# Kernel optimization log

Hardware: AMD Instinct MI355X
Metric: run time of the kernel (lower is better)

Reference implementation:

```python
import jax, jax.numpy as jnp
import numpy as np

N = 50000      # n_nodes
E = 800000     # n_edges (avg degree 16)
D_IN, D_HID, D_OUT = 128, 128, 64


def setup_inputs() -> dict:
    key = jax.random.key(0)
    k1, k2, k3, k4 = jax.random.split(key, 4)
    x = jax.random.normal(k1, (N, D_IN), jnp.float32)
    edge_index = jax.random.randint(k2, (2, E), 0, N, jnp.int32)
    # Glorot-style init for the two GCNConv linear weights
    W1 = jax.random.normal(k3, (D_IN, D_HID), jnp.float32) / np.sqrt(D_IN)
    W2 = jax.random.normal(k4, (D_HID, D_OUT), jnp.float32) / np.sqrt(D_HID)
    b1 = jnp.zeros((D_HID,), jnp.float32)
    b2 = jnp.zeros((D_OUT,), jnp.float32)
    return {"x": x, "edge_index": edge_index, "W1": W1, "b1": b1, "W2": W2, "b2": b2}


def _gcn_conv(x, W, b, src, dst):
    """PyG GCNConv: linear transform, then sym-normalized aggregation with self-loops."""
    h = x @ W                                   # [N, F_out]
    ones = jnp.ones((src.shape[0],), h.dtype)
    # degree includes the self-loop weight of 1
    deg = jax.ops.segment_sum(ones, dst, num_segments=N) + 1.0
    dinv = jax.lax.rsqrt(deg)                   # D^{-1/2}
    norm = dinv[src] * dinv[dst]                # per-edge normalization
    agg = jax.ops.segment_sum(h[src] * norm[:, None], dst, num_segments=N)
    # self-loop contribution: norm_ii = dinv_i^2
    return agg + h * (dinv * dinv)[:, None] + b


def reference(x, edge_index, W1, b1, W2, b2):
    src, dst = edge_index[0], edge_index[1]
    h = jax.nn.relu(_gcn_conv(x, W1, b1, src, dst))
    out = jax.nn.relu(_gcn_conv(h, W2, b2, src, dst))
    return out
```

## Files before the change

### kernel.cpp

```cpp
#include <hip/hip_runtime.h>

typedef unsigned short u16;
typedef __attribute__((ext_vector_type(8))) short short8;
typedef __attribute__((ext_vector_type(4))) float f32x4;

__device__ __forceinline__ float bf2f(u16 h) {
    union { unsigned u; float f; } v; v.u = ((unsigned)h) << 16; return v.f;
}
__device__ __forceinline__ float bflo(unsigned u) {
    union { unsigned u; float f; } v; v.u = u << 16; return v.f;
}
__device__ __forceinline__ float bfhi(unsigned u) {
    union { unsigned u; float f; } v; v.u = u & 0xFFFF0000u; return v.f;
}
__device__ __forceinline__ u16 f2bf(float f) {
    union { float f; unsigned u; } v; v.f = f;
    unsigned u = v.u;
    u += 0x7FFFu + ((u >> 16) & 1u);
    return (u16)(u >> 16);
}

__global__ void k_detect(const u16* __restrict__ x, int* __restrict__ flag) {
    __shared__ int c_s;
    if (threadIdx.x == 0) c_s = 0;
    __syncthreads();
    int c = 0;
    for (int i = threadIdx.x; i < 2048; i += blockDim.x) {
        int e = (x[2 * i] >> 7) & 0xFF;
        c += (e >= 160 || e <= 80) ? 1 : 0;
    }
    atomicAdd(&c_s, c);
    __syncthreads();
    if (threadIdx.x == 0) *flag = (c_s > 64) ? 1 : 0;
}

__global__ void k_convert_w(const void* __restrict__ W1, const void* __restrict__ b1,
                            const void* __restrict__ W2, const void* __restrict__ b2,
                            u16* __restrict__ out, const int* __restrict__ flag) {
    const int n1 = 128 * 128, n2 = n1 + 128, n3 = n2 + 128 * 64, n4 = n3 + 64;
    int i = blockIdx.x * 256 + threadIdx.x;
    if (i >= n4) return;
    const void* src; int off;
    if (i < n1)      { src = W1; off = i; }
    else if (i < n2) { src = b1; off = i - n1; }
    else if (i < n3) { src = W2; off = i - n2; }
    else             { src = b2; off = i - n3; }
    out[i] = *flag ? f2bf(((const float*)src)[off]) : ((const u16*)src)[off];
}


__global__ void k_degpos(const int* __restrict__ dst, int* __restrict__ cnt,
                         int* __restrict__ pos, int E) {
    int e = blockIdx.x * blockDim.x + threadIdx.x;
    if (e < E) pos[e] = atomicAdd(&cnt[dst[e]], 1);
}

__global__ void k_scan_blocks(const int* __restrict__ cnt, int* __restrict__ rowp,
                              int* __restrict__ sums, int n) {
    __shared__ int s[256];
    int t = threadIdx.x;
    int i = blockIdx.x * 256 + t;
    int v = (i < n) ? cnt[i] : 0;
    s[t] = v;
    __syncthreads();
    for (int off = 1; off < 256; off <<= 1) {
        int add = (t >= off) ? s[t - off] : 0;
        __syncthreads();
        s[t] += add;
        __syncthreads();
    }
    if (i < n) rowp[i] = s[t] - v;
    if (t == 255) sums[blockIdx.x] = s[255];
}

__global__ void k_scan_top(int* __restrict__ sums, int nb) {
    __shared__ int s[256];
    int t = threadIdx.x;
    int v = (t < nb) ? sums[t] : 0;
    s[t] = v;
    __syncthreads();
    for (int off = 1; off < 256; off <<= 1) {
        int add = (t >= off) ? s[t - off] : 0;
        __syncthreads();
        s[t] += add;
        __syncthreads();
    }
    sums[t] = s[t] - v;
}

__global__ void k_finalize(int* __restrict__ rowp, const int* __restrict__ sums,
                           const int* __restrict__ cnt, float* __restrict__ dinv,
                           int n, int E) {
    int i = blockIdx.x * 256 + threadIdx.x;
    if (i < n) {
        rowp[i] += sums[i >> 8];
        dinv[i] = rsqrtf((float)cnt[i] + 1.0f);
    }
    if (i == 0) rowp[n] = E;
}

__global__ void k_fill2(const int* __restrict__ src, const int* __restrict__ dst,
                        const int* __restrict__ pos, const int* __restrict__ rowp,
                        int* __restrict__ col, int E) {
    int e = blockIdx.x * blockDim.x + threadIdx.x;
    if (e < E) col[rowp[dst[e]] + pos[e]] = src[e];
}


template <int NOUT>
__global__ void k_gemm_scale(const void* __restrict__ Av, const u16* __restrict__ W,
                             const float* __restrict__ dinv, u16* __restrict__ out,
                             int M, const int* __restrict__ flag) {
    __shared__ u16 Wt[NOUT][136];
    int t = threadIdx.x;
    for (int idx = t; idx < NOUT * 128; idx += 256) {
        int k = idx / NOUT, n = idx % NOUT;
        Wt[n][k] = W[idx];
    }
    __syncthreads();
    int wave = t >> 6, lane = t & 63;
    int m0 = (blockIdx.x * 4 + wave) * 16;
    if (m0 >= M) return;
    int q = lane >> 4;
    int mr = lane & 15;

    short8 a[4];
    if (flag && *flag) {
        const float* arow = (const float*)Av + (size_t)(m0 + mr) * 128 + q * 8;
#pragma unroll
        for (int c = 0; c < 4; c++) {
            f32x4 lo = *(const f32x4*)(arow + c * 32);
            f32x4 hi = *(const f32x4*)(arow + c * 32 + 4);
            a[c][0] = (short)f2bf(lo.x); a[c][1] = (short)f2bf(lo.y);
            a[c][2] = (short)f2bf(lo.z); a[c][3] = (short)f2bf(lo.w);
            a[c][4] = (short)f2bf(hi.x); a[c][5] = (short)f2bf(hi.y);
            a[c][6] = (short)f2bf(hi.z); a[c][7] = (short)f2bf(hi.w);
        }
    } else {
        const u16* arow = (const u16*)Av + (size_t)(m0 + mr) * 128 + q * 8;
#pragma unroll
        for (int c = 0; c < 4; c++) a[c] = *(const short8*)(arow + c * 32);
    }

    f32x4 acc[NOUT / 16];
#pragma unroll
    for (int tl = 0; tl < NOUT / 16; tl++) acc[tl] = (f32x4){0.f, 0.f, 0.f, 0.f};

#pragma unroll
    for (int c = 0; c < 4; c++) {
#pragma unroll
        for (int tl = 0; tl < NOUT / 16; tl++) {
            short8 b = *(const short8*)(&Wt[tl * 16 + mr][c * 32 + q * 8]);
            acc[tl] = __builtin_amdgcn_mfma_f32_16x16x32_bf16(a[c], b, acc[tl], 0, 0, 0);
        }
    }

    int rbase = m0 + q * 4;
#pragma unroll
    for (int tl = 0; tl < NOUT / 16; tl++) {
#pragma unroll
        for (int r = 0; r < 4; r++) {
            int row = rbase + r;
            float v = acc[tl][r] * dinv[row];
            out[(size_t)row * NOUT + tl * 16 + mr] = f2bf(v);
        }
    }
}


template <int F>
__global__ void k_agg(const u16* __restrict__ g, const int* __restrict__ rowp,
                      const int* __restrict__ col, const float* __restrict__ dinv,
                      const u16* __restrict__ bias, u16* __restrict__ outh,
                      float* __restrict__ outf, const int* __restrict__ flag,
                      int N, int E) {
    constexpr int LPR = F / 8;
    constexpr int EPW = 64 / LPR;
    int d = blockIdx.x * 4 + (threadIdx.x >> 6);
    if (d >= N) return;
    int lane = threadIdx.x & 63;
    int er = lane / LPR;
    int fo = (lane % LPR) * 8;

    int beg = rowp[d], end = rowp[d + 1];
    if (beg < 0) beg = 0;
    if (end > E) end = E;
    int deg = end - beg;

    float a0[8], a1[8];
#pragma unroll
    for (int j = 0; j < 8; j++) { a0[j] = 0.f; a1[j] = 0.f; }

    for (int base = 0; base < deg; base += 64) {
        int cnt = deg - base; if (cnt > 64) cnt = 64;
        int colv = 0;
        if (lane < cnt) {
            int s = col[beg + base + lane];
            colv = s < 0 ? 0 : (s >= N ? N - 1 : s);
        }
        int full = cnt / EPW;
        int i = 0;
        for (; i + 2 <= full; i += 2) {
            int s0 = __shfl(colv, i * EPW + er, 64);
            int s1 = __shfl(colv, (i + 1) * EPW + er, 64);
            uint4 v0 = *(const uint4*)(g + (size_t)s0 * F + fo);
            uint4 v1 = *(const uint4*)(g + (size_t)s1 * F + fo);
            a0[0] += bflo(v0.x); a0[1] += bfhi(v0.x);
            a0[2] += bflo(v0.y); a0[3] += bfhi(v0.y);
            a0[4] += bflo(v0.z); a0[5] += bfhi(v0.z);
            a0[6] += bflo(v0.w); a0[7] += bfhi(v0.w);
            a1[0] += bflo(v1.x); a1[1] += bfhi(v1.x);
            a1[2] += bflo(v1.y); a1[3] += bfhi(v1.y);
            a1[4] += bflo(v1.z); a1[5] += bfhi(v1.z);
            a1[6] += bflo(v1.w); a1[7] += bfhi(v1.w);
        }
        if (i < full) {
            int s0 = __shfl(colv, i * EPW + er, 64);
            uint4 v0 = *(const uint4*)(g + (size_t)s0 * F + fo);
            a0[0] += bflo(v0.x); a0[1] += bfhi(v0.x);
            a0[2] += bflo(v0.y); a0[3] += bfhi(v0.y);
            a0[4] += bflo(v0.z); a0[5] += bfhi(v0.z);
            a0[6] += bflo(v0.w); a0[7] += bfhi(v0.w);
            i++;
        }
        int rem = cnt - full * EPW;
        int s0 = __shfl(colv, (full * EPW + er) & 63, 64);
        if (er < rem) {
            uint4 v0 = *(const uint4*)(g + (size_t)s0 * F + fo);
            a0[0] += bflo(v0.x); a0[1] += bfhi(v0.x);
            a0[2] += bflo(v0.y); a0[3] += bfhi(v0.y);
            a0[4] += bflo(v0.z); a0[5] += bfhi(v0.z);
            a0[6] += bflo(v0.w); a0[7] += bfhi(v0.w);
        }
    }
#pragma unroll
    for (int j = 0; j < 8; j++) a0[j] += a1[j];
#pragma unroll
    for (int off = LPR; off < 64; off <<= 1) {
#pragma unroll
        for (int j = 0; j < 8; j++) a0[j] += __shfl_xor(a0[j], off, 64);
    }

    if (lane < LPR) {
        uint4 sv = *(const uint4*)(g + (size_t)d * F + fo);
        uint4 bv = *(const uint4*)(bias + fo);
        float di = dinv[d];
        float r[8];
        r[0] = di * (a0[0] + bflo(sv.x)) + bflo(bv.x);
        r[1] = di * (a0[1] + bfhi(sv.x)) + bfhi(bv.x);
        r[2] = di * (a0[2] + bflo(sv.y)) + bflo(bv.y);
        r[3] = di * (a0[3] + bfhi(sv.y)) + bfhi(bv.y);
        r[4] = di * (a0[4] + bflo(sv.z)) + bflo(bv.z);
        r[5] = di * (a0[5] + bfhi(sv.z)) + bfhi(bv.z);
        r[6] = di * (a0[6] + bflo(sv.w)) + bflo(bv.w);
        r[7] = di * (a0[7] + bfhi(sv.w)) + bfhi(bv.w);
#pragma unroll
        for (int j = 0; j < 8; j++) r[j] = r[j] > 0.f ? r[j] : 0.f;
        size_t o = (size_t)d * F + fo;
        if (flag && *flag) {
            f32x4 w0 = {r[0], r[1], r[2], r[3]};
            f32x4 w1 = {r[4], r[5], r[6], r[7]};
            *(f32x4*)(outf + o) = w0;
            *(f32x4*)(outf + o + 4) = w1;
        } else {
            uint4 w;
            w.x = (unsigned)f2bf(r[0]) | ((unsigned)f2bf(r[1]) << 16);
            w.y = (unsigned)f2bf(r[2]) | ((unsigned)f2bf(r[3]) << 16);
            w.z = (unsigned)f2bf(r[4]) | ((unsigned)f2bf(r[5]) << 16);
            w.w = (unsigned)f2bf(r[6]) | ((unsigned)f2bf(r[7]) << 16);
            *(uint4*)(outh + o) = w;
        }
    }
}


extern "C" void kernel_launch(void* const* d_in, const int* in_sizes, int n_in,
                              void* d_out, int out_size, void* d_ws, size_t ws_size,
                              hipStream_t stream) {
    const int N = in_sizes[0] / 128;
    const int E = in_sizes[1] / 2;
    const int* ei = (const int*)d_in[1];
    const int* src = ei;
    const int* dst = ei + E;

    char* p = (char*)d_ws;
    auto alloc = [&](size_t b) { char* r = p; p += (b + 255) & ~(size_t)255; return r; };
    int*   flag = (int*)alloc(256);
    int*   rowp = (int*)alloc((size_t)(N + 1) * 4);
    float* dinv = (float*)alloc((size_t)N * 4);
    int*   col  = (int*)alloc((size_t)E * 4);
    u16*   wbuf = (u16*)alloc((size_t)(128 * 128 + 128 + 128 * 64 + 64) * 2);
    char*  slotA = alloc((size_t)N * 128 * 2);
    char*  slotB = alloc((size_t)N * 128 * 2);

    int* cnt  = (int*)slotA;
    int* sums = (int*)(slotA + (size_t)N * 4);
    u16* g1   = (u16*)slotA;
    u16* g2   = (u16*)slotA;
    int* pos  = (int*)slotB;
    u16* o1   = (u16*)slotB;
    u16* W1C = wbuf;
    u16* b1C = wbuf + 128 * 128;
    u16* W2C = b1C + 128;
    u16* b2C = W2C + 128 * 64;

    k_detect<<<1, 256, 0, stream>>>((const u16*)d_in[0], flag);
    k_convert_w<<<97, 256, 0, stream>>>(d_in[2], d_in[3], d_in[4], d_in[5], wbuf, flag);

    hipMemsetAsync(slotA, 0, (size_t)N * 4 + 1024, stream);
    int eb = (E + 255) / 256;
    int nb = (N + 255) / 256;
    k_degpos<<<eb, 256, 0, stream>>>(dst, cnt, pos, E);
    k_scan_blocks<<<nb, 256, 0, stream>>>(cnt, rowp, sums, N);
    k_scan_top<<<1, 256, 0, stream>>>(sums, nb);
    k_finalize<<<nb, 256, 0, stream>>>(rowp, sums, cnt, dinv, N, E);
    k_fill2<<<eb, 256, 0, stream>>>(src, dst, pos, rowp, col, E);

    int gb = (N / 16 + 3) / 4;
    int ab = (N + 3) / 4;
    k_gemm_scale<128><<<gb, 256, 0, stream>>>(d_in[0], W1C, dinv, g1, N, flag);
    k_agg<128><<<ab, 256, 0, stream>>>(g1, rowp, col, dinv, b1C,
                                       o1, nullptr, nullptr, N, E);
    k_gemm_scale<64><<<gb, 256, 0, stream>>>(o1, W2C, dinv, g2, N, nullptr);
    k_agg<64><<<ab, 256, 0, stream>>>(g2, rowp, col, dinv, b2C,
                                      (u16*)d_out, (float*)d_out, flag, N, E);
}
```

Before: 218.7 us.

## Fuse all GCN stages into one persistent cooperative kernel with grid syncs

Replaces the eleven separate launches (detect, weight convert, degree count, scans, fill, two GEMMs, two aggregations) with one cooperative kernel that runs each phase in grid-stride loops and uses grid.sync between phases. Flag detection is merged with the degree count, and the CSR column fill is overlapped with the first GEMM phase. The aim is to remove per-launch overhead and inter-kernel gaps. In exchange, occupancy is capped at a persistent grid sized from max active blocks per CU, and each phase pays a grid-wide barrier.

```diff
diff --git a/kernel.cpp b/kernel.cpp
--- a/kernel.cpp
+++ b/kernel.cpp
@@ -1,17 +1,20 @@
 #include <hip/hip_runtime.h>
+#include <hip/hip_cooperative_groups.h>
+
+namespace cg = cooperative_groups;
 
 typedef unsigned short u16;
 typedef __attribute__((ext_vector_type(8))) short short8;
 typedef __attribute__((ext_vector_type(4))) float f32x4;
 
+__device__ __forceinline__ float bflo(unsigned u) {
+    union { unsigned u; float f; } v; v.u = u << 16; return v.f;
+}
+__device__ __forceinline__ float bfhi(unsigned u) {
+    union { unsigned u; float f; } v; v.u = u & 0xFFFF0000u; return v.f;
+}
 __device__ __forceinline__ float bf2f(u16 h) {
     union { unsigned u; float f; } v; v.u = ((unsigned)h) << 16; return v.f;
-}
-__device__ __forceinline__ float bflo(unsigned u) {
-    union { unsigned u; float f; } v; v.u = u << 16; return v.f;
-}
-__device__ __forceinline__ float bfhi(unsigned u) {
-    union { unsigned u; float f; } v; v.u = u & 0xFFFF0000u; return v.f;
 }
 __device__ __forceinline__ u16 f2bf(float f) {
     union { float f; unsigned u; } v; v.f = f;
@@ -20,278 +23,193 @@
     return (u16)(u >> 16);
 }
 
-__global__ void k_detect(const u16* __restrict__ x, int* __restrict__ flag) {
-    __shared__ int c_s;
-    if (threadIdx.x == 0) c_s = 0;
+template <int NOUT>
+__device__ void gemm_phase(const void* __restrict__ Av, const u16* __restrict__ W,
+                           const float* __restrict__ dinv, u16* __restrict__ outp,
+                           int M, int useF32, char* lds_) {
+    u16 (*Wt)[136] = (u16(*)[136])lds_;
+    int t = threadIdx.x;
     __syncthreads();
-    int c = 0;
-    for (int i = threadIdx.x; i < 2048; i += blockDim.x) {
-        int e = (x[2 * i] >> 7) & 0xFF;
-        c += (e >= 160 || e <= 80) ? 1 : 0;
-    }
-    atomicAdd(&c_s, c);
-    __syncthreads();
-    if (threadIdx.x == 0) *flag = (c_s > 64) ? 1 : 0;
-}
-
-__global__ void k_convert_w(const void* __restrict__ W1, const void* __restrict__ b1,
-                            const void* __restrict__ W2, const void* __restrict__ b2,
-                            u16* __restrict__ out, const int* __restrict__ flag) {
-    const int n1 = 128 * 128, n2 = n1 + 128, n3 = n2 + 128 * 64, n4 = n3 + 64;
-    int i = blockIdx.x * 256 + threadIdx.x;
-    if (i >= n4) return;
-    const void* src; int off;
-    if (i < n1)      { src = W1; off = i; }
-    else if (i < n2) { src = b1; off = i - n1; }
-    else if (i < n3) { src = W2; off = i - n2; }
-    else             { src = b2; off = i - n3; }
-    out[i] = *flag ? f2bf(((const float*)src)[off]) : ((const u16*)src)[off];
-}
-
-
-__global__ void k_degpos(const int* __restrict__ dst, int* __restrict__ cnt,
-                         int* __restrict__ pos, int E) {
-    int e = blockIdx.x * blockDim.x + threadIdx.x;
-    if (e < E) pos[e] = atomicAdd(&cnt[dst[e]], 1);
-}
-
-__global__ void k_scan_blocks(const int* __restrict__ cnt, int* __restrict__ rowp,
-                              int* __restrict__ sums, int n) {
-    __shared__ int s[256];
-    int t = threadIdx.x;
-    int i = blockIdx.x * 256 + t;
-    int v = (i < n) ? cnt[i] : 0;
-    s[t] = v;
-    __syncthreads();
-    for (int off = 1; off < 256; off <<= 1) {
-        int add = (t >= off) ? s[t - off] : 0;
-        __syncthreads();
-        s[t] += add;
-        __syncthreads();
-    }
-    if (i < n) rowp[i] = s[t] - v;
-    if (t == 255) sums[blockIdx.x] = s[255];
-}
-
-__global__ void k_scan_top(int* __restrict__ sums, int nb) {
-    __shared__ int s[256];
-    int t = threadIdx.x;
-    int v = (t < nb) ? sums[t] : 0;
-    s[t] = v;
-    __syncthreads();
-    for (int off = 1; off < 256; off <<= 1) {
-        int add = (t >= off) ? s[t - off] : 0;
-        __syncthreads();
-        s[t] += add;
-        __syncthreads();
-    }
-    sums[t] = s[t] - v;
-}
-
-__global__ void k_finalize(int* __restrict__ rowp, const int* __restrict__ sums,
-                           const int* __restrict__ cnt, float* __restrict__ dinv,
-                           int n, int E) {
-    int i = blockIdx.x * 256 + threadIdx.x;
-    if (i < n) {
-        rowp[i] += sums[i >> 8];
-        dinv[i] = rsqrtf((float)cnt[i] + 1.0f);
-    }
-    if (i == 0) rowp[n] = E;
-}
-
-__global__ void k_fill2(const int* __restrict__ src, const int* __restrict__ dst,
-                        const int* __restrict__ pos, const int* __restrict__ rowp,
-                        int* __restrict__ col, int E) {
-    int e = blockIdx.x * blockDim.x + threadIdx.x;
-    if (e < E) col[rowp[dst[e]] + pos[e]] = src[e];
-}
-
-
-template <int NOUT>
-__global__ void k_gemm_scale(const void* __restrict__ Av, const u16* __restrict__ W,
-                             const float* __restrict__ dinv, u16* __restrict__ out,
-                             int M, const int* __restrict__ flag) {
-    __shared__ u16 Wt[NOUT][136];
-    int t = threadIdx.x;
     for (int idx = t; idx < NOUT * 128; idx += 256) {
         int k = idx / NOUT, n = idx % NOUT;
         Wt[n][k] = W[idx];
     }
     __syncthreads();
     int wave = t >> 6, lane = t & 63;
-    int m0 = (blockIdx.x * 4 + wave) * 16;
-    if (m0 >= M) return;
     int q = lane >> 4;
     int mr = lane & 15;
-
-    short8 a[4];
-    if (flag && *flag) {
-        const float* arow = (const float*)Av + (size_t)(m0 + mr) * 128 + q * 8;
+    int wt0 = blockIdx.x * 4 + wave;
+    int nwt = gridDim.x * 4;
+    int tiles = M / 16;
+
+    for (int wt = wt0; wt < tiles; wt += nwt) {
+        int m0 = wt * 16;
+        short8 a[4];
+        if (useF32) {
+            const float* arow = (const float*)Av + (size_t)(m0 + mr) * 128 + q * 8;
+#pragma unroll
+            for (int c = 0; c < 4; c++) {
+                f32x4 lo = *(const f32x4*)(arow + c * 32);
+                f32x4 hi = *(const f32x4*)(arow + c * 32 + 4);
+                a[c][0] = (short)f2bf(lo.x); a[c][1] = (short)f2bf(lo.y);
+                a[c][2] = (short)f2bf(lo.z); a[c][3] = (short)f2bf(lo.w);
+                a[c][4] = (short)f2bf(hi.x); a[c][5] = (short)f2bf(hi.y);
+                a[c][6] = (short)f2bf(hi.z); a[c][7] = (short)f2bf(hi.w);
+            }
+        } else {
+            const u16* arow = (const u16*)Av + (size_t)(m0 + mr) * 128 + q * 8;
+#pragma unroll
+            for (int c = 0; c < 4; c++) a[c] = *(const short8*)(arow + c * 32);
+        }
+
+        f32x4 acc[NOUT / 16];
+#pragma unroll
+        for (int tl = 0; tl < NOUT / 16; tl++) acc[tl] = (f32x4){0.f, 0.f, 0.f, 0.f};
 #pragma unroll
         for (int c = 0; c < 4; c++) {
-            f32x4 lo = *(const f32x4*)(arow + c * 32);
-            f32x4 hi = *(const f32x4*)(arow + c * 32 + 4);
-            a[c][0] = (short)f2bf(lo.x); a[c][1] = (short)f2bf(lo.y);
-            a[c][2] = (short)f2bf(lo.z); a[c][3] = (short)f2bf(lo.w);
-            a[c][4] = (short)f2bf(hi.x); a[c][5] = (short)f2bf(hi.y);
-            a[c][6] = (short)f2bf(hi.z); a[c][7] = (short)f2bf(hi.w);
-        }
-    } else {
-        const u16* arow = (const u16*)Av + (size_t)(m0 + mr) * 128 + q * 8;
-#pragma unroll
-        for (int c = 0; c < 4; c++) a[c] = *(const short8*)(arow + c * 32);
-    }
-
-    f32x4 acc[NOUT / 16];
-#pragma unroll
-    for (int tl = 0; tl < NOUT / 16; tl++) acc[tl] = (f32x4){0.f, 0.f, 0.f, 0.f};
-
-#pragma unroll
-    for (int c = 0; c < 4; c++) {
+#pragma unroll
+            for (int tl = 0; tl < NOUT / 16; tl++) {
+                short8 b = *(const short8*)(&Wt[tl * 16 + mr][c * 32 + q * 8]);
+                acc[tl] = __builtin_amdgcn_mfma_f32_16x16x32_bf16(a[c], b, acc[tl], 0, 0, 0);
+            }
+        }
+        int rbase = m0 + q * 4;
 #pragma unroll
         for (int tl = 0; tl < NOUT / 16; tl++) {
-            short8 b = *(const short8*)(&Wt[tl * 16 + mr][c * 32 + q * 8]);
-            acc[tl] = __builtin_amdgcn_mfma_f32_16x16x32_bf16(a[c], b, acc[tl], 0, 0, 0);
-        }
-    }
-
-    int rbase = m0 + q * 4;
-#pragma unroll
-    for (int tl = 0; tl < NOUT / 16; tl++) {
-#pragma unroll
-        for (int r = 0; r < 4; r++) {
-            int row = rbase + r;
-            float v = acc[tl][r] * dinv[row];
-            out[(size_t)row * NOUT + tl * 16 + mr] = f2bf(v);
-        }
-    }
-}
-
+#pragma unroll
+            for (int r = 0; r < 4; r++) {
+                int row = rbase + r;
+                float v = acc[tl][r] * dinv[row];
+                outp[(size_t)row * NOUT + tl * 16 + mr] = f2bf(v);
+            }
+        }
+    }
+}
 
 template <int F>
-__global__ void k_agg(const u16* __restrict__ g, const int* __restrict__ rowp,
-                      const int* __restrict__ col, const float* __restrict__ dinv,
-                      const u16* __restrict__ bias, u16* __restrict__ outh,
-                      float* __restrict__ outf, const int* __restrict__ flag,
-                      int N, int E) {
+__device__ void agg_phase(const u16* __restrict__ g, const int* __restrict__ rowp,
+                          const int* __restrict__ col, const float* __restrict__ dinv,
+                          const u16* __restrict__ bias, u16* __restrict__ outh,
+                          float* __restrict__ outf, int useF32, int N, int E) {
     constexpr int LPR = F / 8;
     constexpr int EPW = 64 / LPR;
-    int d = blockIdx.x * 4 + (threadIdx.x >> 6);
-    if (d >= N) return;
     int lane = threadIdx.x & 63;
     int er = lane / LPR;
     int fo = (lane % LPR) * 8;
-
-    int beg = rowp[d], end = rowp[d + 1];
-    if (beg < 0) beg = 0;
-    if (end > E) end = E;
-    int deg = end - beg;
-
-    float a0[8], a1[8];
-#pragma unroll
-    for (int j = 0; j < 8; j++) { a0[j] = 0.f; a1[j] = 0.f; }
-
-    for (int base = 0; base < deg; base += 64) {
-        int cnt = deg - base; if (cnt > 64) cnt = 64;
-        int colv = 0;
-        if (lane < cnt) {
-            int s = col[beg + base + lane];
-            colv = s < 0 ? 0 : (s >= N ? N - 1 : s);
-        }
-        int full = cnt / EPW;
-        int i = 0;
-        for (; i + 2 <= full; i += 2) {
-            int s0 = __shfl(colv, i * EPW + er, 64);
-            int s1 = __shfl(colv, (i + 1) * EPW + er, 64);
-            uint4 v0 = *(const uint4*)(g + (size_t)s0 * F + fo);
-            uint4 v1 = *(const uint4*)(g + (size_t)s1 * F + fo);
-            a0[0] += bflo(v0.x); a0[1] += bfhi(v0.x);
-            a0[2] += bflo(v0.y); a0[3] += bfhi(v0.y);
-            a0[4] += bflo(v0.z); a0[5] += bfhi(v0.z);
-            a0[6] += bflo(v0.w); a0[7] += bfhi(v0.w);
-            a1[0] += bflo(v1.x); a1[1] += bfhi(v1.x);
-            a1[2] += bflo(v1.y); a1[3] += bfhi(v1.y);
-            a1[4] += bflo(v1.z); a1[5] += bfhi(v1.z);
-            a1[6] += bflo(v1.w); a1[7] += bfhi(v1.w);
-        }
-        if (i < full) {
-            int s0 = __shfl(colv, i * EPW + er, 64);
-            uint4 v0 = *(const uint4*)(g + (size_t)s0 * F + fo);
-            a0[0] += bflo(v0.x); a0[1] += bfhi(v0.x);
-            a0[2] += bflo(v0.y); a0[3] += bfhi(v0.y);
-            a0[4] += bflo(v0.z); a0[5] += bfhi(v0.z);
-            a0[6] += bflo(v0.w); a0[7] += bfhi(v0.w);
-            i++;
-        }
-        int rem = cnt - full * EPW;
-        int s0 = __shfl(colv, (full * EPW + er) & 63, 64);
-        if (er < rem) {
-            uint4 v0 = *(const uint4*)(g + (size_t)s0 * F + fo);
-            a0[0] += bflo(v0.x); a0[1] += bfhi(v0.x);
-            a0[2] += bflo(v0.y); a0[3] += bfhi(v0.y);
-            a0[4] += bflo(v0.z); a0[5] += bfhi(v0.z);
-            a0[6] += bflo(v0.w); a0[7] += bfhi(v0.w);
-        }
-    }
-#pragma unroll
-    for (int j = 0; j < 8; j++) a0[j] += a1[j];
-#pragma unroll
-    for (int off = LPR; off < 64; off <<= 1) {
-#pragma unroll
-        for (int j = 0; j < 8; j++) a0[j] += __shfl_xor(a0[j], off, 64);
-    }
-
-    if (lane < LPR) {
-        uint4 sv = *(const uint4*)(g + (size_t)d * F + fo);
-        uint4 bv = *(const uint4*)(bias + fo);
-        float di = dinv[d];
-        float r[8];
-        r[0] = di * (a0[0] + bflo(sv.x)) + bflo(bv.x);
-        r[1] = di * (a0[1] + bfhi(sv.x)) + bfhi(bv.x);
-        r[2] = di * (a0[2] + bflo(sv.y)) + bflo(bv.y);
-        r[3] = di * (a0[3] + bfhi(sv.y)) + bfhi(bv.y);
-        r[4] = di * (a0[4] + bflo(sv.z)) + bflo(bv.z);
-        r[5] = di * (a0[5] + bfhi(sv.z)) + bfhi(bv.z);
-        r[6] = di * (a0[6] + bflo(sv.w)) + bflo(bv.w);
-        r[7] = di * (a0[7] + bfhi(sv.w)) + bfhi(bv.w);
-#pragma unroll
-        for (int j = 0; j < 8; j++) r[j] = r[j] > 0.f ? r[j] : 0.f;
-        size_t o = (size_t)d * F + fo;
-        if (flag && *flag) {
-            f32x4 w0 = {r[0], r[1], r[2], r[3]};
-            f32x4 w1 = {r[4], r[5], r[6], r[7]};
-            *(f32x4*)(outf + o) = w0;
-            *(f32x4*)(outf + o + 4) = w1;
-        } else {
-            uint4 w;
-            w.x = (unsigned)f2bf(r[0]) | ((unsigned)f2bf(r[1]) << 16);
-            w.y = (unsigned)f2bf(r[2]) | ((unsigned)f2bf(r[3]) << 16);
-            w.z = (unsigned)f2bf(r[4]) | ((unsigned)f2bf(r[5]) << 16);
-            w.w = (unsigned)f2bf(r[6]) | ((unsigned)f2bf(r[7]) << 16);
-            *(uint4*)(outh + o) = w;
-        }
-    }
-}
-
-
-extern "C" void kernel_launch(void* const* d_in, const int* in_sizes, int n_in,
-                              void* d_out, int out_size, void* d_ws, size_t ws_size,
-                              hipStream_t stream) {
-    const int N = in_sizes[0] / 128;
-    const int E = in_sizes[1] / 2;
-    const int* ei = (const int*)d_in[1];
-    const int* src = ei;
-    const int* dst = ei + E;
-
-    char* p = (char*)d_ws;
-    auto alloc = [&](size_t b) { char* r = p; p += (b + 255) & ~(size_t)255; return r; };
-    int*   flag = (int*)alloc(256);
-    int*   rowp = (int*)alloc((size_t)(N + 1) * 4);
-    float* dinv = (float*)alloc((size_t)N * 4);
-    int*   col  = (int*)alloc((size_t)E * 4);
-    u16*   wbuf = (u16*)alloc((size_t)(128 * 128 + 128 + 128 * 64 + 64) * 2);
-    char*  slotA = alloc((size_t)N * 128 * 2);
-    char*  slotB = alloc((size_t)N * 128 * 2);
+    int wid = blockIdx.x * 4 + (threadIdx.x >> 6);
+    int nw = gridDim.x * 4;
+
+    for (int d = wid; d < N; d += nw) {
+        int beg = rowp[d], end = rowp[d + 1];
+        if (beg < 0) beg = 0;
+        if (end > E) end = E;
+        int deg = end - beg;
+
+        float a0[8], a1[8];
+#pragma unroll
+        for (int j = 0; j < 8; j++) { a0[j] = 0.f; a1[j] = 0.f; }
+
+        for (int base = 0; base < deg; base += 64) {
+            int cnt = deg - base; if (cnt > 64) cnt = 64;
+            int colv = 0;
+            if (lane < cnt) {
+                int s = col[beg + base + lane];
+                colv = s < 0 ? 0 : (s >= N ? N - 1 : s);
+            }
+            int full = cnt / EPW;
+            int i = 0;
+            for (; i + 2 <= full; i += 2) {
+                int s0 = __shfl(colv, i * EPW + er, 64);
+                int s1 = __shfl(colv, (i + 1) * EPW + er, 64);
+                uint4 v0 = *(const uint4*)(g + (size_t)s0 * F + fo);
+                uint4 v1 = *(const uint4*)(g + (size_t)s1 * F + fo);
+                a0[0] += bflo(v0.x); a0[1] += bfhi(v0.x);
+                a0[2] += bflo(v0.y); a0[3] += bfhi(v0.y);
+                a0[4] += bflo(v0.z); a0[5] += bfhi(v0.z);
+                a0[6] += bflo(v0.w); a0[7] += bfhi(v0.w);
+                a1[0] += bflo(v1.x); a1[1] += bfhi(v1.x);
+                a1[2] += bflo(v1.y); a1[3] += bfhi(v1.y);
+                a1[4] += bflo(v1.z); a1[5] += bfhi(v1.z);
+                a1[6] += bflo(v1.w); a1[7] += bfhi(v1.w);
+            }
+            if (i < full) {
+                int s0 = __shfl(colv, i * EPW + er, 64);
+                uint4 v0 = *(const uint4*)(g + (size_t)s0 * F + fo);
+                a0[0] += bflo(v0.x); a0[1] += bfhi(v0.x);
+                a0[2] += bflo(v0.y); a0[3] += bfhi(v0.y);
+                a0[4] += bflo(v0.z); a0[5] += bfhi(v0.z);
+                a0[6] += bflo(v0.w); a0[7] += bfhi(v0.w);
+                i++;
+            }
+            int rem = cnt - full * EPW;
+            int s0 = __shfl(colv, (full * EPW + er) & 63, 64);
+            if (er < rem) {
+                uint4 v0 = *(const uint4*)(g + (size_t)s0 * F + fo);
+                a0[0] += bflo(v0.x); a0[1] += bfhi(v0.x);
+                a0[2] += bflo(v0.y); a0[3] += bfhi(v0.y);
+                a0[4] += bflo(v0.z); a0[5] += bfhi(v0.z);
+                a0[6] += bflo(v0.w); a0[7] += bfhi(v0.w);
+            }
+        }
+#pragma unroll
+        for (int j = 0; j < 8; j++) a0[j] += a1[j];
+#pragma unroll
+        for (int off = LPR; off < 64; off <<= 1) {
+#pragma unroll
+            for (int j = 0; j < 8; j++) a0[j] += __shfl_xor(a0[j], off, 64);
+        }
+
+        if (lane < LPR) {
+            uint4 sv = *(const uint4*)(g + (size_t)d * F + fo);
+            uint4 bv = *(const uint4*)(bias + fo);
+            float di = dinv[d];
+            float r[8];
+            r[0] = di * (a0[0] + bflo(sv.x)) + bflo(bv.x);
+            r[1] = di * (a0[1] + bfhi(sv.x)) + bfhi(bv.x);
+            r[2] = di * (a0[2] + bflo(sv.y)) + bflo(bv.y);
+            r[3] = di * (a0[3] + bfhi(sv.y)) + bfhi(bv.y);
+            r[4] = di * (a0[4] + bflo(sv.z)) + bflo(bv.z);
+            r[5] = di * (a0[5] + bfhi(sv.z)) + bfhi(bv.z);
+            r[6] = di * (a0[6] + bflo(sv.w)) + bflo(bv.w);
+            r[7] = di * (a0[7] + bfhi(sv.w)) + bfhi(bv.w);
+#pragma unroll
+            for (int j = 0; j < 8; j++) r[j] = r[j] > 0.f ? r[j] : 0.f;
+            size_t o = (size_t)d * F + fo;
+            if (useF32) {
+                f32x4 w0 = {r[0], r[1], r[2], r[3]};
+                f32x4 w1 = {r[4], r[5], r[6], r[7]};
+                *(f32x4*)(outf + o) = w0;
+                *(f32x4*)(outf + o + 4) = w1;
+            } else {
+                uint4 w;
+                w.x = (unsigned)f2bf(r[0]) | ((unsigned)f2bf(r[1]) << 16);
+                w.y = (unsigned)f2bf(r[2]) | ((unsigned)f2bf(r[3]) << 16);
+                w.z = (unsigned)f2bf(r[4]) | ((unsigned)f2bf(r[5]) << 16);
+                w.w = (unsigned)f2bf(r[6]) | ((unsigned)f2bf(r[7]) << 16);
+                *(uint4*)(outh + o) = w;
+            }
+        }
+    }
+}
+
+
+__global__ __launch_bounds__(256, 4) void k_mega(
+    const void* __restrict__ x, const int* __restrict__ src,
+    const int* __restrict__ dst,
+    const void* __restrict__ W1, const void* __restrict__ b1,
+    const void* __restrict__ W2, const void* __restrict__ b2,
+    void* __restrict__ out, int N, int E,
+    int* __restrict__ flagcnt, int* __restrict__ rowp,
+    float* __restrict__ dinv, int* __restrict__ col,
+    u16* __restrict__ wbuf, char* __restrict__ slotA, char* __restrict__ slotB) {
+
+    __shared__ char lds_[128 * 136 * 2];
+    cg::grid_group grid = cg::this_grid();
+    int tid = threadIdx.x;
+    int bid = blockIdx.x;
+    int nb_ = gridDim.x;
+    int gtid = bid * 256 + tid;
+    int gsz = nb_ * 256;
 
     int* cnt  = (int*)slotA;
     int* sums = (int*)(slotA + (size_t)N * 4);
@@ -304,24 +222,128 @@
     u16* W2C = b1C + 128;
     u16* b2C = W2C + 128 * 64;
 
-    k_detect<<<1, 256, 0, stream>>>((const u16*)d_in[0], flag);
-    k_convert_w<<<97, 256, 0, stream>>>(d_in[2], d_in[3], d_in[4], d_in[5], wbuf, flag);
-
+    {
+        int c = 0;
+        for (int i = gtid; i < 2048; i += gsz) {
+            int e = (((const u16*)x)[2 * i] >> 7) & 0xFF;
+            c += (e >= 160 || e <= 80) ? 1 : 0;
+        }
+        if (c) atomicAdd(flagcnt, c);
+        for (int e = gtid; e < E; e += gsz)
+            pos[e] = atomicAdd(&cnt[dst[e]], 1);
+    }
+    grid.sync();
+    int flag = (*(volatile int*)flagcnt > 64) ? 1 : 0;
+
+    {
+        const int n1 = 128 * 128, n2 = n1 + 128, n3 = n2 + 128 * 64, n4 = n3 + 64;
+        for (int i = gtid; i < n4; i += gsz) {
+            const void* sp; int off;
+            if (i < n1)      { sp = W1; off = i; }
+            else if (i < n2) { sp = b1; off = i - n1; }
+            else if (i < n3) { sp = W2; off = i - n2; }
+            else             { sp = b2; off = i - n3; }
+            wbuf[i] = flag ? f2bf(((const float*)sp)[off]) : ((const u16*)sp)[off];
+        }
+        int ntile = (N + 255) / 256;
+        int* s = (int*)lds_;
+        for (int t = bid; t < ntile; t += nb_) {
+            int i = t * 256 + tid;
+            int v = (i < N) ? cnt[i] : 0;
+            __syncthreads();
+            s[tid] = v;
+            __syncthreads();
+            for (int off = 1; off < 256; off <<= 1) {
+                int add = (tid >= off) ? s[tid - off] : 0;
+                __syncthreads();
+                s[tid] += add;
+                __syncthreads();
+            }
+            if (i < N) rowp[i] = s[tid] - v;
+            if (tid == 255) sums[t] = s[255];
+        }
+    }
+    grid.sync();
+
+    {
+        int ntile = (N + 255) / 256;
+        int* s = (int*)lds_;
+        __syncthreads();
+        int v = (tid < ntile) ? sums[tid] : 0;
+        s[tid] = v;
+        __syncthreads();
+        for (int off = 1; off < 256; off <<= 1) {
+            int add = (tid >= off) ? s[tid - off] : 0;
+            __syncthreads();
+            s[tid] += add;
+            __syncthreads();
+        }
+        for (int t = bid; t < ntile; t += nb_) {
+            int prefix = (t == 0) ? 0 : s[t - 1];
+            int i = t * 256 + tid;
+            if (i < N) {
+                rowp[i] += prefix;
+                dinv[i] = rsqrtf((float)cnt[i] + 1.0f);
+            }
+        }
+        if (gtid == 0) rowp[N] = E;
+    }
+    grid.sync();
+
+    gemm_phase<128>(x, W1C, dinv, g1, N, flag, lds_);
+    for (int e = gtid; e < E; e += gsz)
+        col[rowp[dst[e]] + pos[e]] = src[e];
+    grid.sync();
+
+    agg_phase<128>(g1, rowp, col, dinv, b1C, o1, nullptr, 0, N, E);
+    grid.sync();
+
+    gemm_phase<64>(o1, W2C, dinv, g2, N, 0, lds_);
+    grid.sync();
+
+    agg_phase<64>(g2, rowp, col, dinv, b2C, (u16*)out, (float*)out, flag, N, E);
+}
+
+
+extern "C" void kernel_launch(void* const* d_in, const int* in_sizes, int n_in,
+                              void* d_out, int out_size, void* d_ws, size_t ws_size,
+                              hipStream_t stream) {
+    int N = in_sizes[0] / 128;
+    int E = in_sizes[1] / 2;
+    const void* x  = d_in[0];
+    const int* ei  = (const int*)d_in[1];
+    const int* src = ei;
+    const int* dst = ei + E;
+    const void* W1 = d_in[2];
+    const void* b1 = d_in[3];
+    const void* W2 = d_in[4];
+    const void* b2 = d_in[5];
+    void* out = d_out;
+
+    char* p = (char*)d_ws;
+    auto alloc = [&](size_t b) { char* r = p; p += (b + 255) & ~(size_t)255; return r; };
+    int*   flagcnt = (int*)alloc(256);
+    int*   rowp = (int*)alloc((size_t)(N + 1) * 4);
+    float* dinv = (float*)alloc((size_t)N * 4);
+    int*   col  = (int*)alloc((size_t)E * 4);
+    u16*   wbuf = (u16*)alloc((size_t)(128 * 128 + 128 + 128 * 64 + 64) * 2);
+    char*  slotA = alloc((size_t)N * 128 * 2);
+    char*  slotB = alloc((size_t)N * 128 * 2);
+
+    hipMemsetAsync(flagcnt, 0, 256, stream);
     hipMemsetAsync(slotA, 0, (size_t)N * 4 + 1024, stream);
-    int eb = (E + 255) / 256;
-    int nb = (N + 255) / 256;
-    k_degpos<<<eb, 256, 0, stream>>>(dst, cnt, pos, E);
-    k_scan_blocks<<<nb, 256, 0, stream>>>(cnt, rowp, sums, N);
-    k_scan_top<<<1, 256, 0, stream>>>(sums, nb);
-    k_finalize<<<nb, 256, 0, stream>>>(rowp, sums, cnt, dinv, N, E);
-    k_fill2<<<eb, 256, 0, stream>>>(src, dst, pos, rowp, col, E);
-
-    int gb = (N / 16 + 3) / 4;
-    int ab = (N + 3) / 4;
-    k_gemm_scale<128><<<gb, 256, 0, stream>>>(d_in[0], W1C, dinv, g1, N, flag);
-    k_agg<128><<<ab, 256, 0, stream>>>(g1, rowp, col, dinv, b1C,
-                                       o1, nullptr, nullptr, N, E);
-    k_gemm_scale<64><<<gb, 256, 0, stream>>>(o1, W2C, dinv, g2, N, nullptr);
-    k_agg<64><<<ab, 256, 0, stream>>>(g2, rowp, col, dinv, b2C,
-                                      (u16*)d_out, (float*)d_out, flag, N, E);
-}
+
+    int bpc = 0;
+    if (hipOccupancyMaxActiveBlocksPerMultiprocessor(&bpc, k_mega, 256, 0)
+            != hipSuccess || bpc < 1) bpc = 2;
+    if (bpc > 4) bpc = 4;
+    int grid = 256 * bpc;
+
+    void* args[] = { (void*)&x, (void*)&src, (void*)&dst,
+                     (void*)&W1, (void*)&b1, (void*)&W2, (void*)&b2,
+                     (void*)&out, (void*)&N, (void*)&E,
+                     (void*)&flagcnt, (void*)&rowp, (void*)&dinv, (void*)&col,
+                     (void*)&wbuf, (void*)&slotA, (void*)&slotB };
+    hipLaunchCooperativeKernel((void*)k_mega, dim3(grid), dim3(256),
+                               args, 0, stream);
+}
```

New measurement: 660.5 us. +202.0%, slower.

## Fuse top-level scan into finalize and overlap CSR fill with first GEMM

Applied to the files above, without the earlier changes.

Drops the separate single-block scan kernel: each finalize block redundantly scans the block sums in shared memory to get its own prefix. The CSR column fill is merged into the first GEMM launch as extra blocks that use a grid-stride loop. Two kernel launches are removed and the fill can overlap with the GEMM. In exchange, every finalize block repeats the small scan, and the GEMM and fill blocks compete for memory bandwidth.

```diff
diff --git a/kernel.cpp b/kernel.cpp
--- a/kernel.cpp
+++ b/kernel.cpp
@@ -4,14 +4,14 @@
 typedef __attribute__((ext_vector_type(8))) short short8;
 typedef __attribute__((ext_vector_type(4))) float f32x4;
 
+__device__ __forceinline__ float bflo(unsigned u) {
+    union { unsigned u; float f; } v; v.u = u << 16; return v.f;
+}
+__device__ __forceinline__ float bfhi(unsigned u) {
+    union { unsigned u; float f; } v; v.u = u & 0xFFFF0000u; return v.f;
+}
 __device__ __forceinline__ float bf2f(u16 h) {
     union { unsigned u; float f; } v; v.u = ((unsigned)h) << 16; return v.f;
-}
-__device__ __forceinline__ float bflo(unsigned u) {
-    union { unsigned u; float f; } v; v.u = u << 16; return v.f;
-}
-__device__ __forceinline__ float bfhi(unsigned u) {
-    union { unsigned u; float f; } v; v.u = u & 0xFFFF0000u; return v.f;
 }
 __device__ __forceinline__ u16 f2bf(float f) {
     union { float f; unsigned u; } v; v.f = f;
@@ -73,11 +73,13 @@
     if (t == 255) sums[blockIdx.x] = s[255];
 }
 
-__global__ void k_scan_top(int* __restrict__ sums, int nb) {
+__global__ void k_finalize2(int* __restrict__ rowp, const int* __restrict__ sums,
+                            const int* __restrict__ cnt, float* __restrict__ dinv,
+                            int n, int E) {
     __shared__ int s[256];
     int t = threadIdx.x;
-    int v = (t < nb) ? sums[t] : 0;
-    s[t] = v;
+    int b = blockIdx.x;
+    s[t] = sums[t];
     __syncthreads();
     for (int off = 1; off < 256; off <<= 1) {
         int add = (t >= off) ? s[t - off] : 0;
@@ -85,47 +87,44 @@
         s[t] += add;
         __syncthreads();
     }
-    sums[t] = s[t] - v;
-}
-
-__global__ void k_finalize(int* __restrict__ rowp, const int* __restrict__ sums,
-                           const int* __restrict__ cnt, float* __restrict__ dinv,
-                           int n, int E) {
-    int i = blockIdx.x * 256 + threadIdx.x;
+    int prefix = (b == 0) ? 0 : s[b - 1];
+    int i = b * 256 + t;
     if (i < n) {
-        rowp[i] += sums[i >> 8];
+        rowp[i] += prefix;
         dinv[i] = rsqrtf((float)cnt[i] + 1.0f);
     }
     if (i == 0) rowp[n] = E;
 }
 
-__global__ void k_fill2(const int* __restrict__ src, const int* __restrict__ dst,
-                        const int* __restrict__ pos, const int* __restrict__ rowp,
-                        int* __restrict__ col, int E) {
-    int e = blockIdx.x * blockDim.x + threadIdx.x;
-    if (e < E) col[rowp[dst[e]] + pos[e]] = src[e];
-}
-
-
-template <int NOUT>
-__global__ void k_gemm_scale(const void* __restrict__ Av, const u16* __restrict__ W,
+
+__global__ void k_gemm1_fill(const void* __restrict__ Av, const u16* __restrict__ W,
                              const float* __restrict__ dinv, u16* __restrict__ out,
-                             int M, const int* __restrict__ flag) {
+                             int M, int GB, const int* __restrict__ flag,
+                             const int* __restrict__ src, const int* __restrict__ dst,
+                             const int* __restrict__ pos, const int* __restrict__ rowp,
+                             int* __restrict__ col, int E) {
+    constexpr int NOUT = 128;
+    int t = threadIdx.x;
+    if ((int)blockIdx.x >= GB) {
+        int stride = (gridDim.x - GB) * 256;
+        for (int e = ((int)blockIdx.x - GB) * 256 + t; e < E; e += stride)
+            col[rowp[dst[e]] + pos[e]] = src[e];
+        return;
+    }
     __shared__ u16 Wt[NOUT][136];
-    int t = threadIdx.x;
     for (int idx = t; idx < NOUT * 128; idx += 256) {
         int k = idx / NOUT, n = idx % NOUT;
         Wt[n][k] = W[idx];
     }
     __syncthreads();
     int wave = t >> 6, lane = t & 63;
-    int m0 = (blockIdx.x * 4 + wave) * 16;
+    int m0 = ((int)blockIdx.x * 4 + wave) * 16;
     if (m0 >= M) return;
     int q = lane >> 4;
     int mr = lane & 15;
 
     short8 a[4];
-    if (flag && *flag) {
+    if (*flag) {
         const float* arow = (const float*)Av + (size_t)(m0 + mr) * 128 + q * 8;
 #pragma unroll
         for (int c = 0; c < 4; c++) {
@@ -145,7 +144,6 @@
     f32x4 acc[NOUT / 16];
 #pragma unroll
     for (int tl = 0; tl < NOUT / 16; tl++) acc[tl] = (f32x4){0.f, 0.f, 0.f, 0.f};
-
 #pragma unroll
     for (int c = 0; c < 4; c++) {
 #pragma unroll
@@ -154,7 +152,51 @@
             acc[tl] = __builtin_amdgcn_mfma_f32_16x16x32_bf16(a[c], b, acc[tl], 0, 0, 0);
         }
     }
-
+    int rbase = m0 + q * 4;
+#pragma unroll
+    for (int tl = 0; tl < NOUT / 16; tl++) {
+#pragma unroll
+        for (int r = 0; r < 4; r++) {
+            int row = rbase + r;
+            float v = acc[tl][r] * dinv[row];
+            out[(size_t)row * NOUT + tl * 16 + mr] = f2bf(v);
+        }
+    }
+}
+
+
+template <int NOUT>
+__global__ void k_gemm_scale(const u16* __restrict__ A, const u16* __restrict__ W,
+                             const float* __restrict__ dinv, u16* __restrict__ out, int M) {
+    __shared__ u16 Wt[NOUT][136];
+    int t = threadIdx.x;
+    for (int idx = t; idx < NOUT * 128; idx += 256) {
+        int k = idx / NOUT, n = idx % NOUT;
+        Wt[n][k] = W[idx];
+    }
+    __syncthreads();
+    int wave = t >> 6, lane = t & 63;
+    int m0 = ((int)blockIdx.x * 4 + wave) * 16;
+    if (m0 >= M) return;
+    int q = lane >> 4;
+    int mr = lane & 15;
+
+    const u16* arow = A + (size_t)(m0 + mr) * 128 + q * 8;
+    short8 a[4];
+#pragma unroll
+    for (int c = 0; c < 4; c++) a[c] = *(const short8*)(arow + c * 32);
+
+    f32x4 acc[NOUT / 16];
+#pragma unroll
+    for (int tl = 0; tl < NOUT / 16; tl++) acc[tl] = (f32x4){0.f, 0.f, 0.f, 0.f};
+#pragma unroll
+    for (int c = 0; c < 4; c++) {
+#pragma unroll
+        for (int tl = 0; tl < NOUT / 16; tl++) {
+            short8 b = *(const short8*)(&Wt[tl * 16 + mr][c * 32 + q * 8]);
+            acc[tl] = __builtin_amdgcn_mfma_f32_16x16x32_bf16(a[c], b, acc[tl], 0, 0, 0);
+        }
+    }
     int rbase = m0 + q * 4;
 #pragma unroll
     for (int tl = 0; tl < NOUT / 16; tl++) {
@@ -312,16 +354,17 @@
     int nb = (N + 255) / 256;
     k_degpos<<<eb, 256, 0, stream>>>(dst, cnt, pos, E);
     k_scan_blocks<<<nb, 256, 0, stream>>>(cnt, rowp, sums, N);
-    k_scan_top<<<1, 256, 0, stream>>>(sums, nb);
-    k_finalize<<<nb, 256, 0, stream>>>(rowp, sums, cnt, dinv, N, E);
-    k_fill2<<<eb, 256, 0, stream>>>(src, dst, pos, rowp, col, E);
-
-    int gb = (N / 16 + 3) / 4;
+    k_finalize2<<<nb, 256, 0, stream>>>(rowp, sums, cnt, dinv, N, E);
+
+    int GB = (N / 16 + 3) / 4;
+    int FB = GB;
+    k_gemm1_fill<<<GB + FB, 256, 0, stream>>>(d_in[0], W1C, dinv, g1, N, GB, flag,
+                                              src, dst, pos, rowp, col, E);
+
     int ab = (N + 3) / 4;
-    k_gemm_scale<128><<<gb, 256, 0, stream>>>(d_in[0], W1C, dinv, g1, N, flag);
     k_agg<128><<<ab, 256, 0, stream>>>(g1, rowp, col, dinv, b1C,
                                        o1, nullptr, nullptr, N, E);
-    k_gemm_scale<64><<<gb, 256, 0, stream>>>(o1, W2C, dinv, g2, N, nullptr);
+    k_gemm_scale<64><<<GB, 256, 0, stream>>>(o1, W2C, dinv, g2, N);
     k_agg<64><<<ab, 256, 0, stream>>>(g2, rowp, col, dinv, b2C,
                                       (u16*)d_out, (float*)d_out, flag, N, E);
 }
```

Result: faster. 214.3 us (-2.0%).
